# Performance work log

Measured on AMD Instinct MI355X. Metric: run time of the kernel, lower is better.

Reference implementation:

```python
import jax, jax.numpy as jnp
import numpy as np
from jax import lax

CIN, COUT, NCLS = 512, 256, 1
B, H, W = 4, 64, 64
EPS = 1e-5


def conv1x1(x, w):
    # x: [B,I,H,W], w: [O,I]
    return jnp.einsum('oi,bihw->bohw', w, x)


def conv3x3(x, w):
    # x: [B,I,H,W], w: [O,I,3,3], padding=1
    return lax.conv_general_dilated(x, w, (1, 1), 'SAME',
                                    dimension_numbers=('NCHW', 'OIHW', 'NCHW'))


def bn_relu(x, g, b):
    # training-mode BatchNorm2d (biased var over B,H,W) + ReLU
    mean = jnp.mean(x, axis=(0, 2, 3), keepdims=True)
    var = jnp.var(x, axis=(0, 2, 3), keepdims=True)
    xn = (x - mean) * lax.rsqrt(var + EPS)
    return jax.nn.relu(xn * g[None, :, None, None] + b[None, :, None, None])


def attention(xf, yf, wq, wk, wv, gamma):
    # cross-attn when yf != xf, self-attn when yf is xf; no 1/sqrt(d) scaling (faithful)
    Bb, C, Hh, Ww = xf.shape
    N = Hh * Ww
    q = conv1x1(xf, wq).reshape(Bb, C, N)
    k = conv1x1(yf, wk).reshape(Bb, C, N)
    v = conv1x1(yf, wv).reshape(Bb, C, N)
    att = jax.nn.softmax(jnp.einsum('bcn,bcm->bnm', q, k), axis=-1)  # [B,N,N]
    out = jnp.einsum('bcm,bnm->bcn', v, att).reshape(Bb, C, Hh, Ww)  # v @ att^T
    return gamma * out + xf


def setup_inputs() -> dict:
    key = jax.random.key(0)
    ks = jax.random.split(key, 16)
    Cs = COUT + 2

    def w(k, shape, fan_in):
        return jax.random.normal(k, shape, dtype=jnp.float32) / np.sqrt(fan_in)

    return {
        'x': jax.random.normal(ks[0], (B, CIN, H, W), dtype=jnp.float32),
        'y': jax.random.normal(ks[1], (B, CIN, H, W), dtype=jnp.float32),
        'flow': jax.random.normal(ks[2], (B, 2, H, W), dtype=jnp.float32),
        'w1x1': w(ks[3], (COUT, CIN), CIN),
        'b1x1': jnp.zeros((COUT,), dtype=jnp.float32),
        'ca_wq': w(ks[4], (COUT, COUT), COUT),
        'ca_wk': w(ks[5], (COUT, COUT), COUT),
        'ca_wv': w(ks[6], (COUT, COUT), COUT),
        'ca_gamma': jnp.full((1,), 0.1, dtype=jnp.float32),
        'cbr1_w': w(ks[7], (COUT, COUT, 3, 3), COUT * 9),
        'bn1_g': jnp.ones((COUT,), dtype=jnp.float32),
        'bn1_b': jnp.zeros((COUT,), dtype=jnp.float32),
        'sa_wq': w(ks[8], (Cs, Cs), Cs),
        'sa_wk': w(ks[9], (Cs, Cs), Cs),
        'sa_wv': w(ks[10], (Cs, Cs), Cs),
        'sa_gamma': jnp.full((1,), 0.1, dtype=jnp.float32),
        'cbr2_w': w(ks[11], (COUT, Cs, 3, 3), Cs * 9),
        'bn2_g': jnp.ones((COUT,), dtype=jnp.float32),
        'bn2_b': jnp.zeros((COUT,), dtype=jnp.float32),
        'pred_w': w(ks[12], (NCLS, COUT), COUT),
        'pred_b': jnp.zeros((NCLS,), dtype=jnp.float32),
    }


def reference(x, y, flow, w1x1, b1x1, ca_wq, ca_wk, ca_wv, ca_gamma,
              cbr1_w, bn1_g, bn1_b, sa_wq, sa_wk, sa_wv, sa_gamma,
              cbr2_w, bn2_g, bn2_b, pred_w, pred_b):
    xb = conv1x1(x, w1x1) + b1x1[None, :, None, None]
    yb = conv1x1(y, w1x1) + b1x1[None, :, None, None]
    t = attention(xb, yb, ca_wq, ca_wk, ca_wv, ca_gamma)
    cross_out = bn_relu(conv3x3(t, cbr1_w), bn1_g, bn1_b)
    cat = jnp.concatenate([cross_out, flow], axis=1)  # [B, COUT+2, H, W]
    t = attention(cat, cat, sa_wq, sa_wk, sa_wv, sa_gamma)
    t = bn_relu(conv3x3(t, cbr2_w), bn2_g, bn2_b)
    out = conv1x1(t, pred_w) + pred_b[None, :, None, None]
    return out
```

## Files before the change

kernel.cpp:

```cpp
#include <hip/hip_runtime.h>
#include <hip/hip_bf16.h>
#include <math.h>


#define NPIX 4096
#define NB   4

typedef __attribute__((ext_vector_type(8))) short short8v;
typedef __attribute__((ext_vector_type(4))) float float4v;

__device__ __forceinline__ short f2bs(float f) {
  __hip_bfloat16 h = __float2bfloat16(f);
  short r; __builtin_memcpy(&r, &h, 2); return r;
}

__device__ __forceinline__ void glld16(const void* g, void* l) {
  __builtin_amdgcn_global_load_lds(
      (const __attribute__((address_space(1))) unsigned int*)g,
      (__attribute__((address_space(3))) unsigned int*)l, 16, 0, 0);
}

__device__ __forceinline__ void vbar() { __builtin_amdgcn_s_barrier(); }

__global__ __launch_bounds__(256) void transp_kernel(
    const float* __restrict__ X, const float* __restrict__ Y,
    __hip_bfloat16* __restrict__ XT, __hip_bfloat16* __restrict__ YT)
{
  const int i0 = blockIdx.x * 64, n0 = blockIdx.y * 64;
  const int z = blockIdx.z, b = z & 3;
  const float* S = (z < 4) ? X : Y;
  __hip_bfloat16* D = (z < 4) ? XT : YT;
  const int tid = threadIdx.x;
  __shared__ float Ls[64][68];
#pragma unroll
  for (int it = 0; it < 4; ++it) {
    int ir = it * 16 + (tid >> 4);
    int nc = (tid & 15) * 4;
    float4 v = *(const float4*)(S + ((size_t)b * 512 + i0 + ir) * NPIX + n0 + nc);
    *(float4*)(&Ls[ir][nc]) = v;
  }
  __syncthreads();
#pragma unroll
  for (int ot = 0; ot < 2; ++ot) {
    int n = ot * 32 + (tid >> 3);
    int ig = tid & 7;
    short8v o;
#pragma unroll
    for (int j = 0; j < 8; ++j) o[j] = f2bs(Ls[8 * ig + j][n]);
    *(short8v*)(D + ((size_t)b * NPIX + n0 + n) * 512 + i0 + 8 * ig) = o;
  }
}

__global__ void wprep_all(
    const float* __restrict__ w1, const float* __restrict__ cq,
    const float* __restrict__ ck, const float* __restrict__ cv,
    const float* __restrict__ sq, const float* __restrict__ sk,
    const float* __restrict__ sv, const float* __restrict__ c1,
    const float* __restrict__ c2,
    __hip_bfloat16* __restrict__ w1o, __hip_bfloat16* __restrict__ cqo,
    __hip_bfloat16* __restrict__ cko, __hip_bfloat16* __restrict__ cvo,
    __hip_bfloat16* __restrict__ sqo, __hip_bfloat16* __restrict__ sko,
    __hip_bfloat16* __restrict__ svo, __hip_bfloat16* __restrict__ c1o,
    __hip_bfloat16* __restrict__ c2o)
{
  const int seg = blockIdx.y;
  const float* src; __hip_bfloat16* dst;
  int Or, Ir, Op, Ip, isconv = 0;
  switch (seg) {
    case 0: src = w1; dst = w1o; Or = 256; Ir = 512; Op = 256; Ip = 512; break;
    case 1: src = cq; dst = cqo; Or = 256; Ir = 256; Op = 256; Ip = 256; break;
    case 2: src = ck; dst = cko; Or = 256; Ir = 256; Op = 256; Ip = 256; break;
    case 3: src = cv; dst = cvo; Or = 256; Ir = 256; Op = 256; Ip = 256; break;
    case 4: src = sq; dst = sqo; Or = 258; Ir = 258; Op = 320; Ip = 288; break;
    case 5: src = sk; dst = sko; Or = 258; Ir = 258; Op = 320; Ip = 288; break;
    case 6: src = sv; dst = svo; Or = 258; Ir = 258; Op = 320; Ip = 288; break;
    case 7: src = c1; dst = c1o; Or = 256; Ir = 256; Op = 256; Ip = 256; isconv = 1; break;
    default: src = c2; dst = c2o; Or = 256; Ir = 258; Op = 256; Ip = 288; isconv = 1; break;
  }
  if (!isconv) {
    size_t total = (size_t)Op * Ip;
    for (size_t e = (size_t)blockIdx.x * 256 + threadIdx.x; e < total;
         e += (size_t)gridDim.x * 256) {
      int i = (int)(e % Ip), o = (int)(e / Ip);
      float v = (o < Or && i < Ir) ? src[(size_t)o * Ir + i] : 0.f;
      dst[e] = __float2bfloat16(v);
    }
  } else {
    size_t total = (size_t)9 * Op * Ip;
    for (size_t e = (size_t)blockIdx.x * 256 + threadIdx.x; e < total;
         e += (size_t)gridDim.x * 256) {
      int i = (int)(e % Ip);
      size_t r = e / Ip;
      int o = (int)(r % Op);
      int dydx = (int)(r / Op);
      float v = (i < Ir) ? src[((size_t)o * Ir + i) * 9 + dydx] : 0.f;
      dst[e] = __float2bfloat16(v);
    }
  }
}

template<int OMODE>
__global__ __launch_bounds__(256, 3) void gemm3_kernel(
    const __hip_bfloat16* __restrict__ X, const __hip_bfloat16* __restrict__ Wb,
    const float* __restrict__ Bias, float* __restrict__ Yf,
    __hip_bfloat16* __restrict__ Yb, int Ip, int O)
{
  const int n0 = blockIdx.x * 64, o0 = blockIdx.y * 64, b = blockIdx.z;
  const int tid = threadIdx.x, wv = tid >> 6, lane = tid & 63;
  const int lg = lane >> 4, lr = lane & 15;
  __shared__ __align__(1024) __hip_bfloat16 Xs[2][64 * 32];
  __shared__ __align__(1024) __hip_bfloat16 Wsh[2][64 * 32];

  const int nn = tid >> 2, ig = tid & 3;
  const __hip_bfloat16* xsrc = X + ((size_t)b * NPIX + n0 + nn) * Ip + 8 * (ig ^ (nn & 3));
  const __hip_bfloat16* wsrc = Wb + (size_t)(o0 + nn) * Ip + 8 * (ig ^ (nn & 3));

  float4v acc[4];
#pragma unroll
  for (int f = 0; f < 4; ++f) acc[f] = (float4v){0.f, 0.f, 0.f, 0.f};

  const int nch = Ip >> 5;

#define GSTAGE(BUF, CI)                            \
  glld16(xsrc + (CI) * 32, &Xs[BUF][tid * 8]);     \
  glld16(wsrc + (CI) * 32, &Wsh[BUF][tid * 8]);

  GSTAGE(0, 0);
  int cur = 0;
  for (int ci = 0; ci < nch; ++ci) {
    asm volatile("s_waitcnt vmcnt(0)" ::: "memory");
    __syncthreads();
    if (ci + 1 < nch) {
      if (cur) { GSTAGE(0, ci + 1); } else { GSTAGE(1, ci + 1); }
    }
    const __hip_bfloat16* xb = &Xs[cur][0];
    const __hip_bfloat16* wb = &Wsh[cur][0];
    if (OMODE != 4) {
      int ar = 16 * wv + lr;
      short8v a = *(const short8v*)(xb + ar * 32 + 8 * (lg ^ (ar & 3)));
#pragma unroll
      for (int of = 0; of < 4; ++of) {
        int br = 16 * of + lr;
        short8v bbv = *(const short8v*)(wb + br * 32 + 8 * (lg ^ (br & 3)));
        acc[of] = __builtin_amdgcn_mfma_f32_16x16x32_bf16(a, bbv, acc[of], 0, 0, 0);
      }
    } else {
      int ar = 16 * wv + lr;
      short8v a = *(const short8v*)(wb + ar * 32 + 8 * (lg ^ (ar & 3)));
#pragma unroll
      for (int nf = 0; nf < 4; ++nf) {
        int br = 16 * nf + lr;
        short8v bbv = *(const short8v*)(xb + br * 32 + 8 * (lg ^ (br & 3)));
        acc[nf] = __builtin_amdgcn_mfma_f32_16x16x32_bf16(a, bbv, acc[nf], 0, 0, 0);
      }
    }
    cur ^= 1;
  }
#undef GSTAGE

  if (OMODE < 2) {
#pragma unroll
    for (int r = 0; r < 4; ++r) {
      size_t row = (size_t)b * NPIX + n0 + 16 * wv + 4 * lg + r;
#pragma unroll
      for (int of = 0; of < 4; ++of) {
        int o = o0 + 16 * of + lr;
        if (o < O) {
          float v = acc[of][r] + (Bias ? Bias[o] : 0.f);
          if (OMODE == 0) Yf[row * O + o] = v;
          Yb[row * O + o] = __float2bfloat16(v);
        }
      }
    }
  } else if (OMODE == 3) {
    __hip_bfloat16* Hb = Yb + (size_t)b * NPIX * O;
#pragma unroll
    for (int r = 0; r < 4; ++r) {
      size_t n = n0 + 16 * wv + 4 * lg + r;
#pragma unroll
      for (int of = 0; of < 4; ++of) {
        int o = o0 + 16 * of + lr;
        if (o < O)
          Hb[((size_t)(o >> 3) * NPIX + n) * 8 + (o & 7)] = __float2bfloat16(acc[of][r]);
      }
    }
  } else {
    __hip_bfloat16* Hb = Yb + (size_t)b * NPIX * O;
#pragma unroll
    for (int r = 0; r < 4; ++r) {
      int c = o0 + 16 * wv + 4 * lg + r;
      if (c < O) {
#pragma unroll
        for (int nf = 0; nf < 4; ++nf) {
          int n = n0 + 16 * nf + lr;
          Hb[((size_t)(n >> 3) * O + c) * 8 + (n & 7)] = __float2bfloat16(acc[nf][r]);
        }
      }
    }
  }
}

template<int C, int RF, int S>
__global__ __launch_bounds__(256, 2) void flash4_kernel(
    const __hip_bfloat16* __restrict__ Q, const __hip_bfloat16* __restrict__ K,
    const __hip_bfloat16* __restrict__ V,
    __hip_bfloat16* __restrict__ Opart, float* __restrict__ ml)
{
  constexpr int N    = NPIX;
  constexpr int NC32 = C / 32;
  constexpr int NCF  = C / 16;
  constexpr int QB   = 16 * RF;
  constexpr int KBYTES = 128 * C;
  constexpr int NT   = (N / S) / 64;

  __shared__ __align__(1024) char smem[256 * C];
  __hip_bfloat16* Ks = (__hip_bfloat16*)smem;
  __hip_bfloat16* Vs = (__hip_bfloat16*)(smem + KBYTES);
  __hip_bfloat16* Ps = (__hip_bfloat16*)smem;

  const int n0 = blockIdx.x * (4 * QB);
  const int split = blockIdx.y, b = blockIdx.z;
  const int tid = threadIdx.x, w = tid >> 6, lane = tid & 63;
  const int lg = lane >> 4, lr = lane & 15;

  const __hip_bfloat16* Kb = K + (size_t)b * N * C;
  const __hip_bfloat16* Vb = V + (size_t)b * N * C;

  short8v qf[RF][NC32];
#pragma unroll
  for (int rf = 0; rf < RF; ++rf) {
    const __hip_bfloat16* qp =
        Q + ((size_t)b * N + n0 + QB * w + 16 * rf + lr) * C + 8 * lg;
#pragma unroll
    for (int ks = 0; ks < NC32; ++ks) qf[rf][ks] = *(const short8v*)(qp + 32 * ks);
  }

  float4v oacc[RF][NCF];
#pragma unroll
  for (int rf = 0; rf < RF; ++rf)
#pragma unroll
    for (int f = 0; f < NCF; ++f) oacc[rf][f] = (float4v){0.f, 0.f, 0.f, 0.f};
  float mrun[RF][4], lrun[RF][4];
#pragma unroll
  for (int rf = 0; rf < RF; ++rf)
#pragma unroll
    for (int r = 0; r < 4; ++r) { mrun[rf][r] = -INFINITY; lrun[rf][r] = 0.f; }

  const int m0base = split * (N / S);

  for (int t = 0; t < NT; ++t) {
    const int m0 = m0base + t * 64;
    __syncthreads();
    for (int u = w; u < C / 8; u += 4)
      glld16(Kb + ((size_t)u * N + m0 + lane) * 8, Ks + u * 512);
    for (int u = w; u < C / 8; u += 4) {
      int s = u * 64 + lane;
      int kv8 = s / C, c = s % C;
      glld16(Vb + ((size_t)(m0 / 8 + kv8) * C + c) * 8, Vs + u * 512);
    }
    asm volatile("s_waitcnt vmcnt(0)" ::: "memory");
    __syncthreads();

    float4v sacc[RF][4];
#pragma unroll
    for (int rf = 0; rf < RF; ++rf)
#pragma unroll
      for (int mf = 0; mf < 4; ++mf) sacc[rf][mf] = (float4v){0.f, 0.f, 0.f, 0.f};
    __builtin_amdgcn_s_setprio(1);
#pragma unroll
    for (int ks = 0; ks < NC32; ++ks)
#pragma unroll
      for (int mf = 0; mf < 4; ++mf) {
        short8v kf = *(const short8v*)(Ks + ((4 * ks + lg) * 64 + 16 * mf + lr) * 8);
#pragma unroll
        for (int rf = 0; rf < RF; ++rf)
          sacc[rf][mf] =
              __builtin_amdgcn_mfma_f32_16x16x32_bf16(qf[rf][ks], kf, sacc[rf][mf], 0, 0, 0);
      }
    __builtin_amdgcn_s_setprio(0);
    __syncthreads();

    float scal[RF][4];
#pragma unroll
    for (int rf = 0; rf < RF; ++rf)
#pragma unroll
      for (int r = 0; r < 4; ++r) {
        float pm = fmaxf(fmaxf(sacc[rf][0][r], sacc[rf][1][r]),
                         fmaxf(sacc[rf][2][r], sacc[rf][3][r]));
#pragma unroll
        for (int off = 1; off < 16; off <<= 1) pm = fmaxf(pm, __shfl_xor(pm, off));
        float mnew = fmaxf(mrun[rf][r], pm);
        float sc = __expf(mrun[rf][r] - mnew);
        mrun[rf][r] = mnew;
        float rs = 0.f;
#pragma unroll
        for (int mf = 0; mf < 4; ++mf) {
          float p = __expf(sacc[rf][mf][r] - mnew);
          rs += p;
          Ps[(size_t)(w * QB + 16 * rf + 4 * lg + r) * 72 + 16 * mf + lr] =
              __float2bfloat16(p);
        }
#pragma unroll
        for (int off = 1; off < 16; off <<= 1) rs += __shfl_xor(rs, off);
        lrun[rf][r] = lrun[rf][r] * sc + rs;
        scal[rf][r] = sc;
      }
#pragma unroll
    for (int rf = 0; rf < RF; ++rf)
#pragma unroll
      for (int f = 0; f < NCF; ++f)
#pragma unroll
        for (int r = 0; r < 4; ++r) oacc[rf][f][r] *= scal[rf][r];

    asm volatile("s_waitcnt lgkmcnt(0)" ::: "memory");

    short8v pa[RF][2];
#pragma unroll
    for (int rf = 0; rf < RF; ++rf)
#pragma unroll
      for (int h = 0; h < 2; ++h)
        pa[rf][h] = *(const short8v*)(Ps + (size_t)(w * QB + 16 * rf + lr) * 72 +
                                      32 * h + 8 * lg);
    __builtin_amdgcn_s_setprio(1);
#pragma unroll
    for (int cf = 0; cf < NCF; ++cf)
#pragma unroll
      for (int h = 0; h < 2; ++h) {
        short8v vf = *(const short8v*)(Vs + ((h * 4 + lg) * C + 16 * cf + lr) * 8);
#pragma unroll
        for (int rf = 0; rf < RF; ++rf)
          oacc[rf][cf] =
              __builtin_amdgcn_mfma_f32_16x16x32_bf16(pa[rf][h], vf, oacc[rf][cf], 0, 0, 0);
      }
    __builtin_amdgcn_s_setprio(0);
  }

  const size_t rbase = (size_t)(split * NB + b) * N;
#pragma unroll
  for (int rf = 0; rf < RF; ++rf)
#pragma unroll
    for (int r = 0; r < 4; ++r) {
      int n = n0 + QB * w + 16 * rf + 4 * lg + r;
      if (lr == 0) {
        ml[(rbase + n) * 2]     = mrun[rf][r];
        ml[(rbase + n) * 2 + 1] = lrun[rf][r];
      }
#pragma unroll
      for (int cf = 0; cf < NCF; ++cf)
        Opart[(rbase + n) * C + 16 * cf + lr] = __float2bfloat16(oacc[rf][cf][r]);
    }
}

template<int C, int S>
__global__ __launch_bounds__(256) void merge4_kernel(
    const __hip_bfloat16* __restrict__ Op, const float* __restrict__ ml,
    const float* __restrict__ R, const float* __restrict__ gamma_p,
    __hip_bfloat16* __restrict__ T)
{
  const size_t row = blockIdx.x;
  float m = -INFINITY;
#pragma unroll
  for (int s = 0; s < S; ++s)
    m = fmaxf(m, ml[((size_t)s * NB * NPIX + row) * 2]);
  float e[S]; float L = 0.f;
#pragma unroll
  for (int s = 0; s < S; ++s) {
    e[s] = __expf(ml[((size_t)s * NB * NPIX + row) * 2] - m);
    L += ml[((size_t)s * NB * NPIX + row) * 2 + 1] * e[s];
  }
  float rinv = gamma_p[0] / L;
  for (int c = threadIdx.x; c < C; c += 256) {
    float o = 0.f;
#pragma unroll
    for (int s = 0; s < S; ++s)
      o += __bfloat162float(Op[((size_t)s * NB * NPIX + row) * C + c]) * e[s];
    T[row * C + c] = __float2bfloat16(o * rinv + R[row * C + c]);
  }
}

template<int IC>
__global__ __launch_bounds__(256, 1) void conv5_kernel(
    const __hip_bfloat16* __restrict__ X, const __hip_bfloat16* __restrict__ W2,
    float* __restrict__ Y)
{
  constexpr int NCH = IC / 32;
  constexpr int XP = 66 * 32;
  const int h0 = blockIdx.x * 4, o0 = blockIdx.y * 64, b = blockIdx.z;
  const int tid = threadIdx.x, wv = tid >> 6, lane = tid & 63;
  const int lg = lane >> 4, lr = lane & 15;

  __shared__ __align__(1024) __hip_bfloat16 Xs[2][6 * XP];
  __shared__ __align__(1024) __hip_bfloat16 Wsh[2][9 * 2048];

  const __hip_bfloat16 zz = __float2bfloat16(0.f);
  for (int e = tid; e < 384; e += 256) {
    int p = e / 64, side = (e >> 5) & 1, ch = e & 31;
    int sl = side ? 65 : 0;
    Xs[0][p * XP + sl * 32 + ch] = zz;
    Xs[1][p * XP + sl * 32 + ch] = zz;
  }
#pragma unroll
  for (int p = 0; p < 6; ++p) {
    int hs = h0 - 1 + p;
    if (hs < 0 || hs > 63) {
      for (int e = tid; e < XP; e += 256) {
        Xs[0][p * XP + e] = zz;
        Xs[1][p * XP + e] = zz;
      }
    }
  }
  __syncthreads();

  float4v acc[4][4];
#pragma unroll
  for (int pf = 0; pf < 4; ++pf)
#pragma unroll
    for (int of = 0; of < 4; ++of) acc[pf][of] = (float4v){0.f, 0.f, 0.f, 0.f};

#define CSTAGE(BUF, CI)                                                        \
  _Pragma("unroll")                                                            \
  for (int k = 0; k < 6; ++k) {                                                \
    int j = wv + k * 4;                                                        \
    int p = j >> 2, seg = j & 3;                                               \
    int hs = h0 - 1 + p;                                                       \
    if (hs >= 0 && hs < 64) {                                                  \
      int px = seg * 16 + (lane >> 2), ig = lane & 3;                          \
      int sl = px + 1;                                                         \
      glld16(X + ((size_t)(b * NPIX + hs * 64 + px)) * IC + (CI) * 32 +        \
                 8 * (ig ^ (sl & 3)),                                          \
             &Xs[BUF][p * XP + (1 + seg * 16) * 32]);                          \
    }                                                                          \
  }                                                                            \
  _Pragma("unroll")                                                            \
  for (int k = 0; k < 9; ++k) {                                                \
    int j = wv + k * 4;                                                        \
    int dydx = j >> 2, seg = j & 3;                                            \
    int oo = seg * 16 + (lane >> 2), ig = lane & 3;                            \
    glld16(W2 + ((size_t)(dydx * 256 + o0 + oo)) * IC + (CI) * 32 +            \
               8 * (ig ^ (oo & 3)),                                            \
           &Wsh[BUF][dydx * 2048 + seg * 512]);                                \
  }

  CSTAGE(0, 0);
  int cur = 0;
  for (int ci = 0; ci < NCH; ++ci) {
    asm volatile("s_waitcnt vmcnt(0) lgkmcnt(0)" ::: "memory");
    vbar();
    __builtin_amdgcn_sched_barrier(0);
    const int cn = (ci + 1 == NCH) ? 0 : ci + 1;
    if (cur) { CSTAGE(0, cn); } else { CSTAGE(1, cn); }
    const __hip_bfloat16* xb = &Xs[cur][0];
    const __hip_bfloat16* wb = &Wsh[cur][0];
    __builtin_amdgcn_s_setprio(1);
#pragma unroll
    for (int dy = 0; dy < 3; ++dy) {
      const __hip_bfloat16* xpl = xb + (wv + dy) * XP;
#pragma unroll
      for (int dx = 0; dx < 3; ++dx) {
        short8v a[4];
#pragma unroll
        for (int pf = 0; pf < 4; ++pf) {
          int sl = pf * 16 + lr + dx;
          a[pf] = *(const short8v*)(xpl + sl * 32 + 8 * (lg ^ (sl & 3)));
        }
#pragma unroll
        for (int of = 0; of < 4; ++of) {
          int br = 16 * of + lr;
          short8v bbv = *(const short8v*)(wb + (dy * 3 + dx) * 2048 + br * 32 +
                                          8 * (lg ^ (br & 3)));
#pragma unroll
          for (int pf = 0; pf < 4; ++pf)
            acc[pf][of] = __builtin_amdgcn_mfma_f32_16x16x32_bf16(a[pf], bbv,
                                                                  acc[pf][of], 0, 0, 0);
        }
      }
    }
    __builtin_amdgcn_s_setprio(0);
    cur ^= 1;
  }
#undef CSTAGE

#pragma unroll
  for (int pf = 0; pf < 4; ++pf)
#pragma unroll
    for (int r = 0; r < 4; ++r) {
      size_t row = (size_t)b * NPIX + (h0 + wv) * 64 + 16 * pf + 4 * lg + r;
#pragma unroll
      for (int of = 0; of < 4; ++of)
        Y[row * 256 + o0 + 16 * of + lr] = acc[pf][of][r];
    }
}

__global__ __launch_bounds__(256) void stats1_kernel(
    const float* __restrict__ X, float* __restrict__ Part)
{
  const int o0 = (blockIdx.x & 3) * 64;
  const int rc = blockIdx.x >> 2;
  const int tid = threadIdx.x;
  const int o = o0 + (tid & 63), rq = tid >> 6;
  float s = 0.f, sq = 0.f;
  for (int rr = rq; rr < 256; rr += 4) {
    float v = X[(size_t)(rc * 256 + rr) * 256 + o];
    s += v; sq += v * v;
  }
  __shared__ float rs[256], rq2[256];
  rs[tid] = s; rq2[tid] = sq;
  __syncthreads();
  if (tid < 64) {
    s  = rs[tid] + rs[tid + 64] + rs[tid + 128] + rs[tid + 192];
    sq = rq2[tid] + rq2[tid + 64] + rq2[tid + 128] + rq2[tid + 192];
    Part[(o0 + tid) * 128 + rc * 2]     = s;
    Part[(o0 + tid) * 128 + rc * 2 + 1] = sq;
  }
}

__global__ __launch_bounds__(256) void stats2_kernel(
    const float* __restrict__ Part, float* __restrict__ Mean, float* __restrict__ Rstd)
{
  const int o = threadIdx.x;
  float s = 0.f, sq = 0.f;
  for (int rc = 0; rc < 64; ++rc) {
    s += Part[o * 128 + rc * 2];
    sq += Part[o * 128 + rc * 2 + 1];
  }
  float mean = s / 16384.f;
  float var = sq / 16384.f - mean * mean;
  Mean[o] = mean;
  Rstd[o] = 1.f / sqrtf(var + 1e-5f);
}

__global__ __launch_bounds__(320) void bnapply1_kernel(
    const float* __restrict__ X, const float* __restrict__ Flow,
    const float* __restrict__ Mean, const float* __restrict__ Rstd,
    const float* __restrict__ G, const float* __restrict__ Bt,
    float* __restrict__ CatF, __hip_bfloat16* __restrict__ CatB)
{
  const size_t row = blockIdx.x;
  const int t = threadIdx.x;
  if (t >= 288) return;
  float val;
  if (t < 256) {
    float v = X[row * 256 + t];
    val = fmaxf((v - Mean[t]) * Rstd[t] * G[t] + Bt[t], 0.f);
  } else if (t < 258) {
    int b = (int)(row >> 12), n = (int)(row & 4095);
    val = Flow[((size_t)(b * 2 + (t - 256)) << 12) + n];
  } else val = 0.f;
  CatF[row * 288 + t] = val;
  CatB[row * 288 + t] = __float2bfloat16(val);
}

__global__ __launch_bounds__(256) void bnpred_kernel(
    const float* __restrict__ X, const float* __restrict__ Mean,
    const float* __restrict__ Rstd, const float* __restrict__ G,
    const float* __restrict__ Bt, const float* __restrict__ Wp,
    const float* __restrict__ Bp, float* __restrict__ Out)
{
  const int wv = threadIdx.x >> 6, lane = threadIdx.x & 63;
  const size_t row = (size_t)blockIdx.x * 4 + wv;
  const float* xr = X + row * 256;
  float acc = 0.f;
#pragma unroll
  for (int cc = 0; cc < 4; ++cc) {
    int c = cc * 64 + lane;
    float v = xr[c];
    v = fmaxf((v - Mean[c]) * Rstd[c] * G[c] + Bt[c], 0.f);
    acc = fmaf(v, Wp[c], acc);
  }
#pragma unroll
  for (int off = 1; off < 64; off <<= 1) acc += __shfl_xor(acc, off);
  if (lane == 0) Out[row] = acc + Bp[0];
}

extern "C" void kernel_launch(void* const* d_in, const int* in_sizes, int n_in,
                              void* d_out, int out_size, void* d_ws, size_t ws_size,
                              hipStream_t stream)
{
  (void)in_sizes; (void)n_in; (void)out_size; (void)ws_size;
  const float* x      = (const float*)d_in[0];
  const float* y      = (const float*)d_in[1];
  const float* flow   = (const float*)d_in[2];
  const float* w1x1   = (const float*)d_in[3];
  const float* b1x1   = (const float*)d_in[4];
  const float* ca_wq  = (const float*)d_in[5];
  const float* ca_wk  = (const float*)d_in[6];
  const float* ca_wv  = (const float*)d_in[7];
  const float* ca_g   = (const float*)d_in[8];
  const float* cbr1_w = (const float*)d_in[9];
  const float* bn1_g  = (const float*)d_in[10];
  const float* bn1_b  = (const float*)d_in[11];
  const float* sa_wq  = (const float*)d_in[12];
  const float* sa_wk  = (const float*)d_in[13];
  const float* sa_wv  = (const float*)d_in[14];
  const float* sa_g   = (const float*)d_in[15];
  const float* cbr2_w = (const float*)d_in[16];
  const float* bn2_g  = (const float*)d_in[17];
  const float* bn2_b  = (const float*)d_in[18];
  const float* pred_w = (const float*)d_in[19];
  const float* pred_b = (const float*)d_in[20];
  float* out = (float*)d_out;

  const size_t FSZ = (size_t)NB * NPIX * 288;
  const size_t SSZ = FSZ / 2;
  float* ws = (float*)d_ws;
  float* F0 = ws;
  float* F1 = ws + FSZ;
  float* F2 = ws + 2 * FSZ;
  float* Sb = ws + 3 * FSZ;
  __hip_bfloat16* S0 = (__hip_bfloat16*)(Sb);
  __hip_bfloat16* S1 = (__hip_bfloat16*)(Sb + SSZ);
  __hip_bfloat16* S2 = (__hip_bfloat16*)(Sb + 2 * SSZ);
  __hip_bfloat16* S3 = (__hip_bfloat16*)(Sb + 3 * SSZ);
  __hip_bfloat16* S4 = (__hip_bfloat16*)(Sb + 4 * SSZ);
  float* Wr = Sb + 5 * SSZ;
  __hip_bfloat16* w1bf  = (__hip_bfloat16*)Wr;
  __hip_bfloat16* caqb  = w1bf + (size_t)256 * 512;
  __hip_bfloat16* cakb  = caqb + (size_t)256 * 256;
  __hip_bfloat16* cavb  = cakb + (size_t)256 * 256;
  __hip_bfloat16* saqb  = cavb + (size_t)256 * 256;
  __hip_bfloat16* sakb  = saqb + (size_t)320 * 288;
  __hip_bfloat16* savb  = sakb + (size_t)320 * 288;
  __hip_bfloat16* w2abf = savb + (size_t)320 * 288;
  __hip_bfloat16* w2bbf = w2abf + (size_t)9 * 256 * 256;
  float* Part = (float*)(w2bbf + (size_t)9 * 256 * 288);
  float* Mean = Part + 32768;
  float* Rstd = Mean + 256;
  float* Mlb  = Rstd + 256;

  __hip_bfloat16* xT = (__hip_bfloat16*)F0;
  __hip_bfloat16* yT = (__hip_bfloat16*)F1;
  __hip_bfloat16* Op = (__hip_bfloat16*)F0;

  dim3 blk(256);

  wprep_all<<<dim3(48, 9), blk, 0, stream>>>(
      w1x1, ca_wq, ca_wk, ca_wv, sa_wq, sa_wk, sa_wv, cbr1_w, cbr2_w,
      w1bf, caqb, cakb, cavb, saqb, sakb, savb, w2abf, w2bbf);

  transp_kernel<<<dim3(8, 64, 8), blk, 0, stream>>>(x, y, xT, yT);

  gemm3_kernel<0><<<dim3(64, 4, 4), blk, 0, stream>>>(xT, w1bf, b1x1, F2, S0, 512, 256);
  gemm3_kernel<1><<<dim3(64, 4, 4), blk, 0, stream>>>(yT, w1bf, b1x1, nullptr, S1, 512, 256);

  gemm3_kernel<1><<<dim3(64, 4, 4), blk, 0, stream>>>(S0, caqb, nullptr, nullptr, S2, 256, 256);
  gemm3_kernel<3><<<dim3(64, 4, 4), blk, 0, stream>>>(S1, cakb, nullptr, nullptr, S3, 256, 256);
  gemm3_kernel<4><<<dim3(64, 4, 4), blk, 0, stream>>>(S1, cavb, nullptr, nullptr, S4, 256, 256);

  flash4_kernel<256, 2, 4><<<dim3(32, 4, 4), blk, 0, stream>>>(S2, S3, S4, Op, Mlb);
  merge4_kernel<256, 4><<<dim3(16384), blk, 0, stream>>>(Op, Mlb, F2, ca_g, S0);

  conv5_kernel<256><<<dim3(16, 4, 4), blk, 0, stream>>>(S0, w2abf, F0);
  stats1_kernel<<<dim3(256), blk, 0, stream>>>(F0, Part);
  stats2_kernel<<<dim3(1), blk, 0, stream>>>(Part, Mean, Rstd);
  bnapply1_kernel<<<dim3(16384), dim3(320), 0, stream>>>(F0, flow, Mean, Rstd,
                                                         bn1_g, bn1_b, F2, S3);

  gemm3_kernel<1><<<dim3(64, 5, 4), blk, 0, stream>>>(S3, saqb, nullptr, nullptr, S0, 288, 288);
  gemm3_kernel<3><<<dim3(64, 5, 4), blk, 0, stream>>>(S3, sakb, nullptr, nullptr, S1, 288, 288);
  gemm3_kernel<4><<<dim3(64, 5, 4), blk, 0, stream>>>(S3, savb, nullptr, nullptr, S2, 288, 288);

  flash4_kernel<288, 1, 2><<<dim3(64, 2, 4), blk, 0, stream>>>(S0, S1, S2, Op, Mlb);
  merge4_kernel<288, 2><<<dim3(16384), blk, 0, stream>>>(Op, Mlb, F2, sa_g, S4);

  conv5_kernel<288><<<dim3(16, 4, 4), blk, 0, stream>>>(S4, w2bbf, F0);
  stats1_kernel<<<dim3(256), blk, 0, stream>>>(F0, Part);
  stats2_kernel<<<dim3(1), blk, 0, stream>>>(Part, Mean, Rstd);
  bnpred_kernel<<<dim3(4096), blk, 0, stream>>>(F0, Mean, Rstd, bn2_g, bn2_b,
                                                pred_w, pred_b, out);
}
```

Before: 507.5 us.

## Enlarge projection GEMM tiles and skip softmax rescale when max stays bounded

The 1x1 projection GEMMs now compute 128-pixel by 64-output tiles with two A fragments per wave, halving the grid and reusing each weight fragment across more MFMAs. In the self-attention flash kernel, a wave-uniform check skips the running-max update and the output accumulator rescale when the new tile's max is within 8 of the running max. This cuts exp and multiply work per KV tile, at the cost of higher register use and lower occupancy in the GEMM, and a slightly larger bf16 P range.

```diff
diff --git a/kernel.cpp b/kernel.cpp
--- a/kernel.cpp
+++ b/kernel.cpp
@@ -100,55 +100,69 @@
 }
 
 template<int OMODE>
-__global__ __launch_bounds__(256, 3) void gemm3_kernel(
+__global__ __launch_bounds__(256, 2) void gemm5_kernel(
     const __hip_bfloat16* __restrict__ X, const __hip_bfloat16* __restrict__ Wb,
     const float* __restrict__ Bias, float* __restrict__ Yf,
     __hip_bfloat16* __restrict__ Yb, int Ip, int O)
 {
-  const int n0 = blockIdx.x * 64, o0 = blockIdx.y * 64, b = blockIdx.z;
+  const int n0 = blockIdx.x * 128, o0 = blockIdx.y * 64, b = blockIdx.z;
   const int tid = threadIdx.x, wv = tid >> 6, lane = tid & 63;
   const int lg = lane >> 4, lr = lane & 15;
-  __shared__ __align__(1024) __hip_bfloat16 Xs[2][64 * 32];
+  __shared__ __align__(1024) __hip_bfloat16 Xs[2][128 * 32];
   __shared__ __align__(1024) __hip_bfloat16 Wsh[2][64 * 32];
 
-  const int nn = tid >> 2, ig = tid & 3;
-  const __hip_bfloat16* xsrc = X + ((size_t)b * NPIX + n0 + nn) * Ip + 8 * (ig ^ (nn & 3));
-  const __hip_bfloat16* wsrc = Wb + (size_t)(o0 + nn) * Ip + 8 * (ig ^ (nn & 3));
-
-  float4v acc[4];
-#pragma unroll
-  for (int f = 0; f < 4; ++f) acc[f] = (float4v){0.f, 0.f, 0.f, 0.f};
-
   const int nch = Ip >> 5;
 
-#define GSTAGE(BUF, CI)                            \
-  glld16(xsrc + (CI) * 32, &Xs[BUF][tid * 8]);     \
-  glld16(wsrc + (CI) * 32, &Wsh[BUF][tid * 8]);
-
-  GSTAGE(0, 0);
+#define G5STAGE(BUF, CI)                                                       \
+  _Pragma("unroll")                                                            \
+  for (int i = 0; i < 2; ++i) {                                                \
+    int u = wv + i * 4;                                                        \
+    int row = 16 * u + (lane >> 2), ig = lane & 3;                             \
+    glld16(X + ((size_t)b * NPIX + n0 + row) * Ip + (CI) * 32 +                \
+               8 * (ig ^ (row & 3)),                                           \
+           &Xs[BUF][u * 512]);                                                 \
+  }                                                                            \
+  {                                                                            \
+    int row = 16 * wv + (lane >> 2), ig = lane & 3;                            \
+    glld16(Wb + (size_t)(o0 + row) * Ip + (CI) * 32 + 8 * (ig ^ (row & 3)),    \
+           &Wsh[BUF][wv * 512]);                                               \
+  }
+
+  float4v acc[8];
+#pragma unroll
+  for (int f = 0; f < 8; ++f) acc[f] = (float4v){0.f, 0.f, 0.f, 0.f};
+
+  G5STAGE(0, 0);
   int cur = 0;
   for (int ci = 0; ci < nch; ++ci) {
     asm volatile("s_waitcnt vmcnt(0)" ::: "memory");
     __syncthreads();
     if (ci + 1 < nch) {
-      if (cur) { GSTAGE(0, ci + 1); } else { GSTAGE(1, ci + 1); }
+      if (cur) { G5STAGE(0, ci + 1); } else { G5STAGE(1, ci + 1); }
     }
     const __hip_bfloat16* xb = &Xs[cur][0];
     const __hip_bfloat16* wb = &Wsh[cur][0];
     if (OMODE != 4) {
-      int ar = 16 * wv + lr;
-      short8v a = *(const short8v*)(xb + ar * 32 + 8 * (lg ^ (ar & 3)));
+      short8v a[2];
+#pragma unroll
+      for (int rf = 0; rf < 2; ++rf) {
+        int ar = 32 * wv + 16 * rf + lr;
+        a[rf] = *(const short8v*)(xb + ar * 32 + 8 * (lg ^ (ar & 3)));
+      }
 #pragma unroll
       for (int of = 0; of < 4; ++of) {
         int br = 16 * of + lr;
         short8v bbv = *(const short8v*)(wb + br * 32 + 8 * (lg ^ (br & 3)));
-        acc[of] = __builtin_amdgcn_mfma_f32_16x16x32_bf16(a, bbv, acc[of], 0, 0, 0);
+#pragma unroll
+        for (int rf = 0; rf < 2; ++rf)
+          acc[rf * 4 + of] =
+              __builtin_amdgcn_mfma_f32_16x16x32_bf16(a[rf], bbv, acc[rf * 4 + of], 0, 0, 0);
       }
     } else {
       int ar = 16 * wv + lr;
       short8v a = *(const short8v*)(wb + ar * 32 + 8 * (lg ^ (ar & 3)));
 #pragma unroll
-      for (int nf = 0; nf < 4; ++nf) {
+      for (int nf = 0; nf < 8; ++nf) {
         int br = 16 * nf + lr;
         short8v bbv = *(const short8v*)(xb + br * 32 + 8 * (lg ^ (br & 3)));
         acc[nf] = __builtin_amdgcn_mfma_f32_16x16x32_bf16(a, bbv, acc[nf], 0, 0, 0);
@@ -156,34 +170,38 @@
     }
     cur ^= 1;
   }
-#undef GSTAGE
+#undef G5STAGE
 
   if (OMODE < 2) {
 #pragma unroll
-    for (int r = 0; r < 4; ++r) {
-      size_t row = (size_t)b * NPIX + n0 + 16 * wv + 4 * lg + r;
-#pragma unroll
-      for (int of = 0; of < 4; ++of) {
-        int o = o0 + 16 * of + lr;
-        if (o < O) {
-          float v = acc[of][r] + (Bias ? Bias[o] : 0.f);
-          if (OMODE == 0) Yf[row * O + o] = v;
-          Yb[row * O + o] = __float2bfloat16(v);
+    for (int rf = 0; rf < 2; ++rf)
+#pragma unroll
+      for (int r = 0; r < 4; ++r) {
+        size_t row = (size_t)b * NPIX + n0 + 32 * wv + 16 * rf + 4 * lg + r;
+#pragma unroll
+        for (int of = 0; of < 4; ++of) {
+          int o = o0 + 16 * of + lr;
+          if (o < O) {
+            float v = acc[rf * 4 + of][r] + (Bias ? Bias[o] : 0.f);
+            if (OMODE == 0) Yf[row * O + o] = v;
+            Yb[row * O + o] = __float2bfloat16(v);
+          }
         }
       }
-    }
   } else if (OMODE == 3) {
     __hip_bfloat16* Hb = Yb + (size_t)b * NPIX * O;
 #pragma unroll
-    for (int r = 0; r < 4; ++r) {
-      size_t n = n0 + 16 * wv + 4 * lg + r;
-#pragma unroll
-      for (int of = 0; of < 4; ++of) {
-        int o = o0 + 16 * of + lr;
-        if (o < O)
-          Hb[((size_t)(o >> 3) * NPIX + n) * 8 + (o & 7)] = __float2bfloat16(acc[of][r]);
-      }
-    }
+    for (int rf = 0; rf < 2; ++rf)
+#pragma unroll
+      for (int r = 0; r < 4; ++r) {
+        size_t n = n0 + 32 * wv + 16 * rf + 4 * lg + r;
+#pragma unroll
+        for (int of = 0; of < 4; ++of) {
+          int o = o0 + 16 * of + lr;
+          if (o < O)
+            Hb[((size_t)(o >> 3) * NPIX + n) * 8 + (o & 7)] = __float2bfloat16(acc[rf * 4 + of][r]);
+        }
+      }
   } else {
     __hip_bfloat16* Hb = Yb + (size_t)b * NPIX * O;
 #pragma unroll
@@ -191,7 +209,7 @@
       int c = o0 + 16 * wv + 4 * lg + r;
       if (c < O) {
 #pragma unroll
-        for (int nf = 0; nf < 4; ++nf) {
+        for (int nf = 0; nf < 8; ++nf) {
           int n = n0 + 16 * nf + lr;
           Hb[((size_t)(n >> 3) * O + c) * 8 + (n & 7)] = __float2bfloat16(acc[nf][r]);
         }
@@ -200,7 +218,7 @@
   }
 }
 
-template<int C, int RF, int S>
+template<int C, int RF, int S, int DM>
 __global__ __launch_bounds__(256, 2) void flash4_kernel(
     const __hip_bfloat16* __restrict__ Q, const __hip_bfloat16* __restrict__ K,
     const __hip_bfloat16* __restrict__ V,
@@ -280,37 +298,73 @@
     __builtin_amdgcn_s_setprio(0);
     __syncthreads();
 
-    float scal[RF][4];
+    float pmx[RF][4];
 #pragma unroll
     for (int rf = 0; rf < RF; ++rf)
 #pragma unroll
       for (int r = 0; r < 4; ++r) {
-        float pm = fmaxf(fmaxf(sacc[rf][0][r], sacc[rf][1][r]),
-                         fmaxf(sacc[rf][2][r], sacc[rf][3][r]));
-#pragma unroll
-        for (int off = 1; off < 16; off <<= 1) pm = fmaxf(pm, __shfl_xor(pm, off));
-        float mnew = fmaxf(mrun[rf][r], pm);
-        float sc = __expf(mrun[rf][r] - mnew);
-        mrun[rf][r] = mnew;
-        float rs = 0.f;
-#pragma unroll
-        for (int mf = 0; mf < 4; ++mf) {
-          float p = __expf(sacc[rf][mf][r] - mnew);
-          rs += p;
-          Ps[(size_t)(w * QB + 16 * rf + 4 * lg + r) * 72 + 16 * mf + lr] =
-              __float2bfloat16(p);
+        float p = fmaxf(fmaxf(sacc[rf][0][r], sacc[rf][1][r]),
+                        fmaxf(sacc[rf][2][r], sacc[rf][3][r]));
+#pragma unroll
+        for (int off = 1; off < 16; off <<= 1) p = fmaxf(p, __shfl_xor(p, off));
+        pmx[rf][r] = p;
+      }
+    bool fast = false;
+    if constexpr (DM) {
+      int myok = 1;
+#pragma unroll
+      for (int rf = 0; rf < RF; ++rf)
+#pragma unroll
+        for (int r = 0; r < 4; ++r)
+          myok &= (pmx[rf][r] <= mrun[rf][r] + 8.f) ? 1 : 0;
+      fast = (__all(myok) != 0);
+    }
+    if (fast) {
+#pragma unroll
+      for (int rf = 0; rf < RF; ++rf)
+#pragma unroll
+        for (int r = 0; r < 4; ++r) {
+          float rs = 0.f;
+#pragma unroll
+          for (int mf = 0; mf < 4; ++mf) {
+            float p = __expf(sacc[rf][mf][r] - mrun[rf][r]);
+            rs += p;
+            Ps[(size_t)(w * QB + 16 * rf + 4 * lg + r) * 72 + 16 * mf + lr] =
+                __float2bfloat16(p);
+          }
+#pragma unroll
+          for (int off = 1; off < 16; off <<= 1) rs += __shfl_xor(rs, off);
+          lrun[rf][r] += rs;
         }
-#pragma unroll
-        for (int off = 1; off < 16; off <<= 1) rs += __shfl_xor(rs, off);
-        lrun[rf][r] = lrun[rf][r] * sc + rs;
-        scal[rf][r] = sc;
-      }
-#pragma unroll
-    for (int rf = 0; rf < RF; ++rf)
-#pragma unroll
-      for (int f = 0; f < NCF; ++f)
-#pragma unroll
-        for (int r = 0; r < 4; ++r) oacc[rf][f][r] *= scal[rf][r];
+    } else {
+      float scal[RF][4];
+#pragma unroll
+      for (int rf = 0; rf < RF; ++rf)
+#pragma unroll
+        for (int r = 0; r < 4; ++r) {
+          float mnew = fmaxf(mrun[rf][r], pmx[rf][r]);
+          float sc = __expf(mrun[rf][r] - mnew);
+          mrun[rf][r] = mnew;
+          float rs = 0.f;
+#pragma unroll
+          for (int mf = 0; mf < 4; ++mf) {
+            float p = __expf(sacc[rf][mf][r] - mnew);
+            rs += p;
+            Ps[(size_t)(w * QB + 16 * rf + 4 * lg + r) * 72 + 16 * mf + lr] =
+                __float2bfloat16(p);
+          }
+#pragma unroll
+          for (int off = 1; off < 16; off <<= 1) rs += __shfl_xor(rs, off);
+          lrun[rf][r] = lrun[rf][r] * sc + rs;
+          scal[rf][r] = sc;
+        }
+#pragma unroll
+      for (int rf = 0; rf < RF; ++rf)
+#pragma unroll
+        for (int f = 0; f < NCF; ++f)
+#pragma unroll
+          for (int r = 0; r < 4; ++r) oacc[rf][f][r] *= scal[rf][r];
+    }
 
     asm volatile("s_waitcnt lgkmcnt(0)" ::: "memory");
 
@@ -639,14 +693,14 @@
 
   transp_kernel<<<dim3(8, 64, 8), blk, 0, stream>>>(x, y, xT, yT);
 
-  gemm3_kernel<0><<<dim3(64, 4, 4), blk, 0, stream>>>(xT, w1bf, b1x1, F2, S0, 512, 256);
-  gemm3_kernel<1><<<dim3(64, 4, 4), blk, 0, stream>>>(yT, w1bf, b1x1, nullptr, S1, 512, 256);
-
-  gemm3_kernel<1><<<dim3(64, 4, 4), blk, 0, stream>>>(S0, caqb, nullptr, nullptr, S2, 256, 256);
-  gemm3_kernel<3><<<dim3(64, 4, 4), blk, 0, stream>>>(S1, cakb, nullptr, nullptr, S3, 256, 256);
-  gemm3_kernel<4><<<dim3(64, 4, 4), blk, 0, stream>>>(S1, cavb, nullptr, nullptr, S4, 256, 256);
-
-  flash4_kernel<256, 2, 4><<<dim3(32, 4, 4), blk, 0, stream>>>(S2, S3, S4, Op, Mlb);
+  gemm5_kernel<0><<<dim3(32, 4, 4), blk, 0, stream>>>(xT, w1bf, b1x1, F2, S0, 512, 256);
+  gemm5_kernel<1><<<dim3(32, 4, 4), blk, 0, stream>>>(yT, w1bf, b1x1, nullptr, S1, 512, 256);
+
+  gemm5_kernel<1><<<dim3(32, 4, 4), blk, 0, stream>>>(S0, caqb, nullptr, nullptr, S2, 256, 256);
+  gemm5_kernel<3><<<dim3(32, 4, 4), blk, 0, stream>>>(S1, cakb, nullptr, nullptr, S3, 256, 256);
+  gemm5_kernel<4><<<dim3(32, 4, 4), blk, 0, stream>>>(S1, cavb, nullptr, nullptr, S4, 256, 256);
+
+  flash4_kernel<256, 2, 4, 0><<<dim3(32, 4, 4), blk, 0, stream>>>(S2, S3, S4, Op, Mlb);
   merge4_kernel<256, 4><<<dim3(16384), blk, 0, stream>>>(Op, Mlb, F2, ca_g, S0);
 
   conv5_kernel<256><<<dim3(16, 4, 4), blk, 0, stream>>>(S0, w2abf, F0);
@@ -655,11 +709,11 @@
   bnapply1_kernel<<<dim3(16384), dim3(320), 0, stream>>>(F0, flow, Mean, Rstd,
                                                          bn1_g, bn1_b, F2, S3);
 
-  gemm3_kernel<1><<<dim3(64, 5, 4), blk, 0, stream>>>(S3, saqb, nullptr, nullptr, S0, 288, 288);
-  gemm3_kernel<3><<<dim3(64, 5, 4), blk, 0, stream>>>(S3, sakb, nullptr, nullptr, S1, 288, 288);
-  gemm3_kernel<4><<<dim3(64, 5, 4), blk, 0, stream>>>(S3, savb, nullptr, nullptr, S2, 288, 288);
-
-  flash4_kernel<288, 1, 2><<<dim3(64, 2, 4), blk, 0, stream>>>(S0, S1, S2, Op, Mlb);
+  gemm5_kernel<1><<<dim3(32, 5, 4), blk, 0, stream>>>(S3, saqb, nullptr, nullptr, S0, 288, 288);
+  gemm5_kernel<3><<<dim3(32, 5, 4), blk, 0, stream>>>(S3, sakb, nullptr, nullptr, S1, 288, 288);
+  gemm5_kernel<4><<<dim3(32, 5, 4), blk, 0, stream>>>(S3, savb, nullptr, nullptr, S2, 288, 288);
+
+  flash4_kernel<288, 1, 2, 1><<<dim3(64, 2, 4), blk, 0, stream>>>(S0, S1, S2, Op, Mlb);
   merge4_kernel<288, 2><<<dim3(16384), blk, 0, stream>>>(Op, Mlb, F2, sa_g, S4);
 
   conv5_kernel<288><<<dim3(16, 4, 4), blk, 0, stream>>>(S4, w2bbf, F0);
```

New measurement: 581.6 us. 1.15x slower.
